# Optimization experiments

Hardware: AMD Instinct MI355X
Metric: run time of the kernel (lower is better)

The kernel has to match this reference:

```python
import jax, jax.numpy as jnp
import numpy as np

E, C, H, W = 64, 8, 32, 32  # E zonotope rows (1 center + 63 error terms)


def setup_inputs() -> dict:
    key = jax.random.key(0)
    x = jax.random.normal(key, (E, C, H, W), dtype=jnp.float32)
    # Zero center => lower < 0 < upper everywhere, so every element crosses
    # and the number of new error terms equals C*H*W (fixed output shape).
    x = x.at[0].set(0.0)
    return {"x": x}


def reference(x):
    e = x.shape[0]
    content_shape = x.shape[1:]
    n = int(np.prod(content_shape))  # max possible new error terms

    err = jnp.sum(jnp.abs(x[1:]), axis=0)
    upper = x[0] + err
    lower = x[0] - err

    cross = (lower * upper < 0).astype(x.dtype)   # crossing-zero mask
    nonneg = (lower >= 0).astype(x.dtype)         # strictly positive mask

    lam = nonneg + cross * upper / (upper - lower)
    lam = jnp.where(jnp.isnan(lam), 0.5, lam)
    # torch assigns lambda via .data (detached from the autograd graph)
    lam = jax.lax.stop_gradient(lam)

    delta = jnp.maximum(-lam * lower, (1.0 - lam) * upper)

    head = (delta / 2 + lam * x[0]) * cross + x[0] * nonneg          # new center
    body = x[1:] * (lam * cross + nonneg)                            # scaled old error terms

    # Vectorized stream-compaction scatter replacing the scripted .item() loop:
    # element k (flat order) with cross==True goes to tail row cumsum(cross)[k]-1.
    flat_cond = cross.reshape(-1) > 0
    vals = (delta / 2).reshape(-1)
    rows = jnp.cumsum(flat_cond.astype(jnp.int32)) - 1
    rows = jnp.clip(rows, 0, n - 1)
    tail = jnp.zeros((n, n), dtype=x.dtype)
    # (row, col) pairs are unique per column; masked-out elements write 0 (no-op).
    tail = tail.at[rows, jnp.arange(n)].set(jnp.where(flat_cond, vals, 0.0))

    return jnp.concatenate(
        [head[None], body, tail.reshape((n,) + content_shape)], axis=0
    )
```

## Files before the change

kernel.cpp:

```cpp
#include <hip/hip_runtime.h>
#include <math.h>

#define EROWS 64
#define NCOL  8192
#define TAIL_OFF (EROWS * NCOL)

__global__ void headbody_kernel(const float* __restrict__ x,
                                float* __restrict__ out,
                                float* __restrict__ val,
                                int* __restrict__ flag) {
    int k = blockIdx.x * blockDim.x + threadIdx.x;
    if (k >= NCOL) return;

    float err = 0.f;
    for (int e = 1; e < EROWS; ++e)
        err += fabsf(x[e * NCOL + k]);

    float x0    = x[k];
    float upper = x0 + err;
    float lower = x0 - err;

    float cross  = (lower * upper < 0.f) ? 1.f : 0.f;
    float nonneg = (lower >= 0.f) ? 1.f : 0.f;

    float lam = nonneg + cross * upper / (upper - lower);
    if (isnan(lam)) lam = 0.5f;

    float delta = fmaxf(-lam * lower, (1.f - lam) * upper);

    out[k] = (delta * 0.5f + lam * x0) * cross + x0 * nonneg;

    float scale = lam * cross + nonneg;
    val[k]  = delta * 0.5f;
    flag[k] = (cross > 0.f) ? 1 : 0;

    for (int e = 1; e < EROWS; ++e)
        out[e * NCOL + k] = x[e * NCOL + k] * scale;
}

__global__ void scatter_kernel(const float* __restrict__ val,
                               const int* __restrict__ flag,
                               float* __restrict__ out) {
    const int t = threadIdx.x;
    const int PER = NCOL / 1024;

    int f[PER];
    int s = 0;
    for (int j = 0; j < PER; ++j) {
        f[j] = flag[t * PER + j];
        s += f[j];
    }

    __shared__ int sh[1024];
    sh[t] = s;
    __syncthreads();

    for (int off = 1; off < 1024; off <<= 1) {
        int v = (t >= off) ? sh[t - off] : 0;
        __syncthreads();
        sh[t] += v;
        __syncthreads();
    }
    int running = (t == 0) ? 0 : sh[t - 1];

    for (int j = 0; j < PER; ++j) {
        int k = t * PER + j;
        if (f[j]) {
            out[TAIL_OFF + (size_t)running * NCOL + k] = val[k];
            ++running;
        }
    }
}

extern "C" void kernel_launch(void* const* d_in, const int* in_sizes, int n_in,
                              void* d_out, int out_size, void* d_ws, size_t ws_size,
                              hipStream_t stream) {
    const float* x = (const float*)d_in[0];
    float* out = (float*)d_out;

    float* val  = (float*)d_ws;
    int*   flag = (int*)((char*)d_ws + NCOL * sizeof(float));

    hipMemsetAsync(d_out, 0, (size_t)out_size * sizeof(float), stream);

    headbody_kernel<<<NCOL / 256, 256, 0, stream>>>(x, out, val, flag);
    scatter_kernel<<<1, 1024, 0, stream>>>(val, flag, out);
}
```

Measured before the change: 275.3 us.

## Replace full-output memset plus scattered writes with dense float4 tail writer

```diff
diff --git a/kernel.cpp b/kernel.cpp
--- a/kernel.cpp
+++ b/kernel.cpp
@@ -4,6 +4,14 @@
 #define EROWS 64
 #define NCOL  8192
 #define TAIL_OFF (EROWS * NCOL)
+#define TAIL_F4 (NCOL * NCOL / 4)
+#define ROW_F4  (NCOL / 4)
+
+#define WS_VAL(ws)     ((float*)(ws))
+#define WS_FLAG(ws)    ((int*)((char*)(ws) + 32768))
+#define WS_COLOF(ws)   ((int*)((char*)(ws) + 65536))
+#define WS_TAILVAL(ws) ((float*)((char*)(ws) + 98304))
+#define WS_COUNT(ws)   ((int*)((char*)(ws) + 131072))
 
 __global__ void headbody_kernel(const float* __restrict__ x,
                                 float* __restrict__ out,
@@ -38,9 +46,11 @@
         out[e * NCOL + k] = x[e * NCOL + k] * scale;
 }
 
-__global__ void scatter_kernel(const float* __restrict__ val,
-                               const int* __restrict__ flag,
-                               float* __restrict__ out) {
+__global__ void scan_kernel(const float* __restrict__ val,
+                            const int* __restrict__ flag,
+                            int* __restrict__ colof,
+                            float* __restrict__ tailval,
+                            int* __restrict__ count) {
     const int t = threadIdx.x;
     const int PER = NCOL / 1024;
 
@@ -66,10 +76,33 @@
     for (int j = 0; j < PER; ++j) {
         int k = t * PER + j;
         if (f[j]) {
-            out[TAIL_OFF + (size_t)running * NCOL + k] = val[k];
+            colof[running]   = k;
+            tailval[running] = val[k];
             ++running;
         }
     }
+    if (t == 1023) *count = sh[1023];
+}
+
+__global__ void tail_kernel(const int* __restrict__ colof,
+                            const float* __restrict__ tailval,
+                            const int* __restrict__ count,
+                            float* __restrict__ out) {
+    int q  = blockIdx.x * blockDim.x + threadIdx.x;
+    int r  = q >> 11;
+    int c0 = (q & 2047) << 2;
+
+    int cnt = *count;
+    int   col = (r < cnt) ? colof[r]   : -1;
+    float tv  = (r < cnt) ? tailval[r] : 0.f;
+
+    float4 v;
+    v.x = (col == c0 + 0) ? tv : 0.f;
+    v.y = (col == c0 + 1) ? tv : 0.f;
+    v.z = (col == c0 + 2) ? tv : 0.f;
+    v.w = (col == c0 + 3) ? tv : 0.f;
+
+    ((float4*)out)[TAIL_OFF / 4 + q] = v;
 }
 
 extern "C" void kernel_launch(void* const* d_in, const int* in_sizes, int n_in,
@@ -78,11 +111,9 @@
     const float* x = (const float*)d_in[0];
     float* out = (float*)d_out;
 
-    float* val  = (float*)d_ws;
-    int*   flag = (int*)((char*)d_ws + NCOL * sizeof(float));
-
-    hipMemsetAsync(d_out, 0, (size_t)out_size * sizeof(float), stream);
-
-    headbody_kernel<<<NCOL / 256, 256, 0, stream>>>(x, out, val, flag);
-    scatter_kernel<<<1, 1024, 0, stream>>>(val, flag, out);
+    headbody_kernel<<<NCOL / 256, 256, 0, stream>>>(x, out, WS_VAL(d_ws), WS_FLAG(d_ws));
+    scan_kernel<<<1, 1024, 0, stream>>>(WS_VAL(d_ws), WS_FLAG(d_ws),
+                                        WS_COLOF(d_ws), WS_TAILVAL(d_ws), WS_COUNT(d_ws));
+    tail_kernel<<<TAIL_F4 / 256, 256, 0, stream>>>(WS_COLOF(d_ws), WS_TAILVAL(d_ws),
+                                                   WS_COUNT(d_ws), out);
 }
```

New measurement: 271.9 us. No clear change (-1.3%).
